# Kernel optimization log

Measured on AMD Instinct MI355X. Metric: run time of the kernel, lower is better.

The kernel has to match this reference:

```python
import jax, jax.numpy as jnp
import numpy as np

B, C, H, W = 8, 64, 200, 320
N = 48            # bboxes (table rows) per image
STRIDE = 4        # pad_w / W
WD = W // STRIDE  # kernel-branch width after downsampling


def setup_inputs() -> dict:
    key = jax.random.key(0)
    ks = jax.random.split(key, 10)
    feats = jax.random.normal(ks[0], (B, C, H, W), dtype=jnp.float32)
    kernel_feats = jax.random.normal(ks[1], (B, C, H, WD), dtype=jnp.float32)
    Wk = jax.random.normal(ks[2], (C + 1, C), dtype=jnp.float32) * 0.05
    bk = jax.random.normal(ks[3], (C + 1,), dtype=jnp.float32) * 0.05
    Wf = jax.random.normal(ks[4], (C, C), dtype=jnp.float32) * 0.05
    bf = jax.random.normal(ks[5], (C,), dtype=jnp.float32) * 0.05
    # bboxes in padded-image pixels; only y1,y2 matter for line_type='row'.
    yc_idx = jax.random.randint(ks[6], (B, N), 0, H).astype(jnp.float32)
    y1 = yc_idx * STRIDE
    y2 = y1  # center = y coordinate exactly on a feature row
    x1 = jnp.zeros((B, N), jnp.float32)
    x2 = jnp.full((B, N), float(W * STRIDE), jnp.float32)
    det_bboxes = jnp.stack([x1, y1, x2, y2], axis=-1)  # [B,N,4]
    image_shape = jax.random.randint(ks[7], (B, 2), 400, 800).astype(jnp.int32)  # [img_w,img_h]
    return {
        "feats": feats, "kernel_feats": kernel_feats,
        "Wk": Wk, "bk": bk, "Wf": Wf, "bf": bf,
        "det_bboxes": det_bboxes, "image_shape": image_shape, "pad_w": 1280,
    }


def reference(feats, kernel_feats, Wk, bk, Wf, bf, det_bboxes, image_shape, pad_w):
    b, c, h, w = feats.shape
    stride = pad_w / w  # 4.0
    # kernel_conv (1x1) then mean over width (line_type='row')
    kernels = jnp.einsum('oc,bchw->bohw', Wk, kernel_feats) + bk[None, :, None, None]
    kernels = kernels.mean(-1)                         # [B, C+1, H]
    # feats_conv (1x1)
    f = jnp.einsum('oc,bchw->bohw', Wf, feats) + bf[None, :, None, None]
    # valid-region masks from per-image (img_w, img_h)
    hlim = (image_shape[:, 1].astype(jnp.float32) / stride).astype(jnp.int32)
    wlim = (image_shape[:, 0].astype(jnp.float32) / stride).astype(jnp.int32)
    mask = (jnp.arange(h)[None, :, None] < hlim[:, None, None]) & \
           (jnp.arange(w)[None, None, :] < wlim[:, None, None])   # [B,H,W]
    # gather per-bbox dynamic kernels at row centers
    yc = (det_bboxes[..., 1] + det_bboxes[..., 3]) / (2.0 * stride)  # [B,N]
    idx = yc.astype(jnp.int32)
    vk = kernels[jnp.arange(b)[:, None], :, idx]       # [B,N,C+1]
    wgt, bias = vk[..., :c], vk[..., c]
    # grouped 1x1 conv == per-instance matvec over channels
    logits = jnp.einsum('bnc,bchw->bnhw', wgt, f) + bias[..., None, None]
    logits = jnp.where(mask[:, None, :, :], logits, jnp.float32(-1e8))
    centers = (yc * stride)[..., None]                 # [B,N,1]
    return logits, centers
```

## Files before the change

### kernel.cpp

```cpp
#include <hip/hip_runtime.h>

#define Bb 8
#define Cc 64
#define Hh 200
#define Ww 320
#define Nn 48
#define WDd 80

__global__ __launch_bounds__(64) void prep_kernel(
    const float* __restrict__ kf, const float* __restrict__ Wk,
    const float* __restrict__ bk, const float* __restrict__ Wf,
    const float* __restrict__ bf, const float* __restrict__ db,
    const int* __restrict__ pad_w,
    float* __restrict__ weffT, float* __restrict__ beff,
    float* __restrict__ centers)
{
    const int n = blockIdx.x, b = blockIdx.y, tid = threadIdx.x;
    const float stride = (float)pad_w[0] / (float)Ww;
    const float yc = (db[(b*Nn + n)*4 + 1] + db[(b*Nn + n)*4 + 3]) / (2.0f * stride);
    const int idx = (int)yc;

    __shared__ float kfm[Cc];
    __shared__ float vk[Cc + 1];

    const float* row = kf + ((size_t)(b*Cc + tid)*Hh + idx)*WDd;
    float s = 0.f;
    #pragma unroll
    for (int w0 = 0; w0 < WDd; ++w0) s += row[w0];
    kfm[tid] = s * (1.0f / (float)WDd);
    __syncthreads();

    {
        float a = bk[tid];
        #pragma unroll 8
        for (int c = 0; c < Cc; ++c) a = fmaf(Wk[tid*Cc + c], kfm[c], a);
        vk[tid] = a;
        if (tid == 0) {
            float a2 = bk[Cc];
            for (int c = 0; c < Cc; ++c) a2 = fmaf(Wk[Cc*Cc + c], kfm[c], a2);
            vk[Cc] = a2;
        }
    }
    __syncthreads();

    float wsum = 0.f;
    #pragma unroll 8
    for (int c = 0; c < Cc; ++c) wsum = fmaf(vk[c], Wf[c*Cc + tid], wsum);
    weffT[((size_t)b*Cc + tid)*Nn + n] = wsum;

    if (tid == 0) {
        float bb2 = vk[Cc];
        for (int c = 0; c < Cc; ++c) bb2 = fmaf(vk[c], bf[c], bb2);
        beff[b*Nn + n] = bb2;
        centers[b*Nn + n] = yc * stride;
    }
}

__global__ __launch_bounds__(64) void logits_kernel(
    const float* __restrict__ feats, const int* __restrict__ ishape,
    const int* __restrict__ pad_w, const float* __restrict__ weffT,
    const float* __restrict__ beff, float* __restrict__ out)
{
    const int b = blockIdx.z;
    const int h = blockIdx.y;
    const int w = blockIdx.x * 64 + threadIdx.x;

    const float stride = (float)pad_w[0] / (float)Ww;
    const int hlim = (int)((float)ishape[b*2 + 1] / stride);
    const int wlim = (int)((float)ishape[b*2 + 0] / stride);
    const bool act = (h < hlim) && (w < wlim);

    float acc[Nn];
    if (__ballot(act) != 0ULL) {
        const float* __restrict__ bv = beff + b*Nn;
        #pragma unroll
        for (int n = 0; n < Nn; ++n) acc[n] = bv[n];

        const float* __restrict__ fp = feats + ((size_t)(b*Cc)*Hh + h)*Ww + w;
        const float* __restrict__ wT = weffT + (size_t)b*Cc*Nn;
        #pragma unroll 4
        for (int c = 0; c < Cc; ++c) {
            const float fv = fp[(size_t)c * (Hh*Ww)];
            const float* __restrict__ wrow = wT + c*Nn;
            #pragma unroll
            for (int n = 0; n < Nn; ++n) acc[n] = fmaf(wrow[n], fv, acc[n]);
        }
    } else {
        #pragma unroll
        for (int n = 0; n < Nn; ++n) acc[n] = -1e8f;
    }

    float* op = out + ((size_t)(b*Nn)*Hh + h)*Ww + w;
    #pragma unroll
    for (int n = 0; n < Nn; ++n)
        op[(size_t)n * (Hh*Ww)] = act ? acc[n] : -1e8f;
}

extern "C" void kernel_launch(void* const* d_in, const int* in_sizes, int n_in,
                              void* d_out, int out_size, void* d_ws, size_t ws_size,
                              hipStream_t stream) {
    const float* feats  = (const float*)d_in[0];
    const float* kf     = (const float*)d_in[1];
    const float* Wk     = (const float*)d_in[2];
    const float* bk     = (const float*)d_in[3];
    const float* Wf     = (const float*)d_in[4];
    const float* bf     = (const float*)d_in[5];
    const float* db     = (const float*)d_in[6];
    const int*   ishape = (const int*)d_in[7];
    const int*   pad_w  = (const int*)d_in[8];

    float* out    = (float*)d_out;
    float* weffT  = (float*)d_ws;
    float* beff   = weffT + (size_t)Bb*Cc*Nn;
    float* centers = out + (size_t)Bb*Nn*Hh*Ww;

    prep_kernel<<<dim3(Nn, Bb), 64, 0, stream>>>(
        kf, Wk, bk, Wf, bf, db, pad_w, weffT, beff, centers);

    logits_kernel<<<dim3(Ww/64, Hh, Bb), 64, 0, stream>>>(
        feats, ishape, pad_w, weffT, beff, out);
}
```

Measured before the change: 248.8 us.

## Coalesce prep loads via shared memory, enlarge logits blocks, use nontemporal stores

The prep kernel now loads kernel-feature rows and the Wk matrix in a coalesced way into padded shared memory, and replaces serial single-thread dot products with wave shuffle reductions. The logits kernel moves from 64 to 256 threads per block, with each block covering four rows. Its 98 MB output is written with nontemporal stores so the streaming writes do not pollute the cache. This adds shared-memory use in prep, and the larger blocks change occupancy for a kernel that already holds many registers.

```diff
diff --git a/kernel.cpp b/kernel.cpp
--- a/kernel.cpp
+++ b/kernel.cpp
@@ -20,26 +20,43 @@
     const float yc = (db[(b*Nn + n)*4 + 1] + db[(b*Nn + n)*4 + 3]) / (2.0f * stride);
     const int idx = (int)yc;
 
+    __shared__ float buf[65*65];
     __shared__ float kfm[Cc];
     __shared__ float vk[Cc + 1];
 
-    const float* row = kf + ((size_t)(b*Cc + tid)*Hh + idx)*WDd;
-    float s = 0.f;
-    #pragma unroll
-    for (int w0 = 0; w0 < WDd; ++w0) s += row[w0];
-    kfm[tid] = s * (1.0f / (float)WDd);
+    const float* __restrict__ kfb = kf + ((size_t)b*Cc*Hh + idx)*WDd;
+    #pragma unroll 4
+    for (int c = 0; c < Cc; ++c) {
+        const float* __restrict__ p = kfb + (size_t)c*Hh*WDd;
+        float v = p[tid];
+        if (tid < (WDd - 64)) v += p[64 + tid];
+        buf[c*65 + tid] = v;
+    }
     __syncthreads();
 
     {
+        float s = 0.f;
+        #pragma unroll 8
+        for (int j = 0; j < Cc; ++j) s += buf[tid*65 + j];
+        kfm[tid] = s * (1.0f / (float)WDd);
+    }
+    __syncthreads();
+
+    for (int g = tid; g < 65*Cc; g += 64)
+        buf[g + (g >> 6)] = Wk[g];
+    __syncthreads();
+
+    const float kfm_t = kfm[tid];
+    {
         float a = bk[tid];
         #pragma unroll 8
-        for (int c = 0; c < Cc; ++c) a = fmaf(Wk[tid*Cc + c], kfm[c], a);
+        for (int c = 0; c < Cc; ++c) a = fmaf(buf[tid*65 + c], kfm[c], a);
         vk[tid] = a;
-        if (tid == 0) {
-            float a2 = bk[Cc];
-            for (int c = 0; c < Cc; ++c) a2 = fmaf(Wk[Cc*Cc + c], kfm[c], a2);
-            vk[Cc] = a2;
-        }
+
+        float e = buf[64*65 + tid] * kfm_t;
+        #pragma unroll
+        for (int off = 32; off > 0; off >>= 1) e += __shfl_down(e, off);
+        if (tid == 0) vk[Cc] = e + bk[Cc];
     }
     __syncthreads();
 
@@ -48,22 +65,24 @@
     for (int c = 0; c < Cc; ++c) wsum = fmaf(vk[c], Wf[c*Cc + tid], wsum);
     weffT[((size_t)b*Cc + tid)*Nn + n] = wsum;
 
+    float e2 = vk[tid] * bf[tid];
+    #pragma unroll
+    for (int off = 32; off > 0; off >>= 1) e2 += __shfl_down(e2, off);
     if (tid == 0) {
-        float bb2 = vk[Cc];
-        for (int c = 0; c < Cc; ++c) bb2 = fmaf(vk[c], bf[c], bb2);
-        beff[b*Nn + n] = bb2;
+        beff[b*Nn + n] = e2 + vk[Cc];
         centers[b*Nn + n] = yc * stride;
     }
 }
 
-__global__ __launch_bounds__(64) void logits_kernel(
+__global__ __launch_bounds__(256) void logits_kernel(
     const float* __restrict__ feats, const int* __restrict__ ishape,
     const int* __restrict__ pad_w, const float* __restrict__ weffT,
     const float* __restrict__ beff, float* __restrict__ out)
 {
     const int b = blockIdx.z;
-    const int h = blockIdx.y;
-    const int w = blockIdx.x * 64 + threadIdx.x;
+    const int h = blockIdx.y * 4 + (threadIdx.x >> 6);
+    const int lane = threadIdx.x & 63;
+    const int w = blockIdx.x * 64 + lane;
 
     const float stride = (float)pad_w[0] / (float)Ww;
     const int hlim = (int)((float)ishape[b*2 + 1] / stride);
@@ -93,7 +112,7 @@
     float* op = out + ((size_t)(b*Nn)*Hh + h)*Ww + w;
     #pragma unroll
     for (int n = 0; n < Nn; ++n)
-        op[(size_t)n * (Hh*Ww)] = act ? acc[n] : -1e8f;
+        __builtin_nontemporal_store(act ? acc[n] : -1e8f, op + (size_t)n * (Hh*Ww));
 }
 
 extern "C" void kernel_launch(void* const* d_in, const int* in_sizes, int n_in,
@@ -117,6 +136,6 @@
     prep_kernel<<<dim3(Nn, Bb), 64, 0, stream>>>(
         kf, Wk, bk, Wf, bf, db, pad_w, weffT, beff, centers);
 
-    logits_kernel<<<dim3(Ww/64, Hh, Bb), 64, 0, stream>>>(
+    logits_kernel<<<dim3(Ww/64, Hh/4, Bb), 256, 0, stream>>>(
         feats, ishape, pad_w, weffT, beff, out);
 }
```

Result: slower. 270.0 us (+8.5%).
